# Performance work log

Hardware: AMD Instinct MI355X
Metric: run time of the kernel (lower is better)

Reference implementation:

```python
import jax, jax.numpy as jnp
import numpy as np

B, C, H = 2, 32, 64  # batch, base channel, bottleneck spatial size
EPS = 1e-5


def _conv(x, w, b, pad):
    # standard NCHW conv, stride 1
    out = jax.lax.conv_general_dilated(x, w, (1, 1), [(pad, pad), (pad, pad)],
                                       dimension_numbers=("NCHW", "OIHW", "NCHW"))
    return out + b[None, :, None, None]


def _inorm(x):
    # InstanceNorm2d, affine=False (torch default)
    m = jnp.mean(x, axis=(2, 3), keepdims=True)
    v = jnp.var(x, axis=(2, 3), keepdims=True)
    return (x - m) * jax.lax.rsqrt(v + EPS)


def _patches3(x):
    # x: (B,C,H,W) -> (B,C,9,H-2,W-2); 3x3 patches, stride 1, VALID
    oh, ow = x.shape[-2] - 2, x.shape[-1] - 2
    return jnp.stack([x[:, :, i:i + oh, j:j + ow] for i in range(3) for j in range(3)], axis=2)


def _pac_kernel(g):
    # gaussian pixel-adaptive kernel (NVlabs/pac, kernel_type='gaussian', normalize_kernel=False)
    # g: (B,Cg,H,W) -> K: (B,9,H,W), K = exp(-0.5*||f_nbr - f_center||^2)
    gp = jnp.pad(g, ((0, 0), (0, 0), (1, 1), (1, 1)))
    p = _patches3(gp)                      # (B,Cg,9,H,W)
    d = p - g[:, :, None]                  # center is offset (1,1) == g itself
    return jnp.exp(-0.5 * jnp.sum(d * d, axis=1))


def _pacconvT(x, g, w, b):
    # PacConvTranspose2d: kernel_size=3, stride=2, padding=1, output_padding=1
    # native impl: zero-upsample, pad (k-1)-p=1 left/top and 1+out_pad=2 right/bottom,
    # then pixel-adaptive conv with weight.permute(1,0,2,3) (no spatial flip, per PAC).
    Bc, Cin, Hh, Ww = x.shape
    z = jnp.zeros((Bc, Cin, 2 * Hh - 1, 2 * Ww - 1), x.dtype).at[:, :, ::2, ::2].set(x)
    z = jnp.pad(z, ((0, 0), (0, 0), (1, 2), (1, 2)))
    p = _patches3(z)                       # (B,Cin,9,2H,2W)
    k = _pac_kernel(g)                     # (B,9,2H,2W)
    wf = jnp.transpose(w, (1, 0, 2, 3)).reshape(w.shape[1], w.shape[0], 9)  # (Cout,Cin,9)
    out = jnp.einsum('bckhw,bkhw,ock->bohw', p, k, wf)
    return out + b[None, :, None, None]


def _w(key, shape, scale):
    return jax.random.normal(key, shape, dtype=jnp.float32) * scale


def setup_inputs():
    key = jax.random.key(0)
    ks = jax.random.split(key, 20)
    return {
        "x": jax.random.normal(ks[0], (B, 8 * C, H, H), jnp.float32),
        "ef_lv2": jax.random.normal(ks[1], (B, 2 * C, 2 * H, 2 * H), jnp.float32),
        "ef_lv1": jax.random.normal(ks[2], (B, C, 4 * H, 4 * H), jnp.float32),
        "W_down": _w(ks[3], (4 * C, 8 * C, 3, 3), (8 * C * 9) ** -0.5),
        "b_down": _w(ks[4], (4 * C,), 0.01),
        "W_mid": _w(ks[5], (4 * C, 4 * C, 1, 1), (4 * C) ** -0.5),
        "b_mid": _w(ks[6], (4 * C,), 0.01),
        "W_adj2": _w(ks[7], (4 * C, 2 * C, 3, 3), 0.002),  # small: keeps gaussian kernel non-degenerate
        "b_adj2": _w(ks[8], (4 * C,), 0.01),
        "W_adj1": _w(ks[9], (2 * C, C, 3, 3), 0.004),
        "b_adj1": _w(ks[10], (2 * C,), 0.01),
        "W16": _w(ks[11], (4 * C, 2 * C, 3, 3), (4 * C * 9) ** -0.5),  # convT layout (Cin,Cout,kh,kw)
        "b16": _w(ks[12], (2 * C,), 0.01),
        "W20": _w(ks[13], (2 * C, C, 3, 3), (2 * C * 9) ** -0.5),
        "b20": _w(ks[14], (C,), 0.01),
        "W24": _w(ks[15], (3, C, 3, 3), (C * 9) ** -0.5),
        "b24": _w(ks[16], (3,), 0.01),
    }


def reference(x, ef_lv2, ef_lv1, W_down, b_down, W_mid, b_mid, W_adj2, b_adj2,
              W_adj1, b_adj1, W16, b16, W20, b20, W24, b24):
    x = _conv(_inorm(x), W_down, b_down, 1)          # layer13: norm + channel-down 8C->4C
    x = _conv(x, W_mid, b_mid, 0) + x                # middle_layer13 1x1 + residual
    g2 = _conv(ef_lv2, W_adj2, b_adj2, 1)            # adjust_ef_lv2 2C->4C
    x = _pacconvT(x, g2, W16, b16)                   # layer16: 4C->2C, x2 spatial
    x = _inorm(x) + x                                # layer17 + residual (twice)
    x = _inorm(x) + x
    g1 = _conv(ef_lv1, W_adj1, b_adj1, 1)            # adjust_ef_lv1 C->2C
    x = _pacconvT(x, g1, W20, b20)                   # layer20: 2C->C, x2 spatial
    x = _inorm(x) + x                                # layer21 + residual (twice)
    x = _inorm(x) + x
    return _conv(x, W24, b24, 1)                     # layer24: C->3
```

## Files before the change

### kernel.cpp

```cpp
#include <hip/hip_runtime.h>

#define EPS 1e-5f

typedef short sh8 __attribute__((ext_vector_type(8)));
typedef float f32x4 __attribute__((ext_vector_type(4)));

__device__ __forceinline__ ushort f2b(float f) {
    unsigned u = __float_as_uint(f);
    u += 0x7fffu + ((u >> 16) & 1u);
    return (ushort)(u >> 16);
}
__device__ __forceinline__ float b2f(ushort u) {
    return __uint_as_float((unsigned)u << 16);
}

__device__ __forceinline__ void istat_body(int ch, const float* __restrict__ in,
                                           float* st, int HW)
{
    __shared__ double sh[512];
    const float* p = in + (size_t)ch * HW;
    double s = 0.0, s2 = 0.0;
    for (int i = threadIdx.x * 4; i < HW; i += 1024) {
        float4 v = *(const float4*)(p + i);
        s  += (double)v.x + (double)v.y + (double)v.z + (double)v.w;
        s2 += (double)v.x * v.x + (double)v.y * v.y
            + (double)v.z * v.z + (double)v.w * v.w;
    }
    sh[threadIdx.x] = s; sh[256 + threadIdx.x] = s2;
    __syncthreads();
    for (int o = 128; o > 0; o >>= 1) {
        if ((int)threadIdx.x < o) {
            sh[threadIdx.x]       += sh[threadIdx.x + o];
            sh[256 + threadIdx.x] += sh[256 + threadIdx.x + o];
        }
        __syncthreads();
    }
    if (threadIdx.x == 0) {
        double m = sh[0] / (double)HW;
        double v = sh[256] / (double)HW - m * m;
        st[2 * ch]     = (float)m;
        st[2 * ch + 1] = (float)(v < 0.0 ? 0.0 : v);
    }
}

__device__ __forceinline__ void ipad_body(int bxi, int b,
    const float* __restrict__ in, const float* __restrict__ st,
    ushort* __restrict__ ob, int C, int H, int W, int pad, int n4)
{
    int idx = bxi * 256 + threadIdx.x;
    if (idx >= n4) return;
    int cpp = C >> 2;
    int pp = idx / cpp, c0 = (idx - pp * cpp) * 4;
    int Wp = W + 2 * pad, Hp = H + 2 * pad;
    int yp = pp / Wp, xp = pp - yp * Wp;
    int y = yp - pad, x = xp - pad;
    ushort4 o;
    if (y >= 0 && y < H && x >= 0 && x < W) {
        size_t HW = (size_t)H * W;
        const float* ib = in + (size_t)b * C * HW + (size_t)y * W + x;
        #pragma unroll
        for (int u = 0; u < 4; u++) {
            int chg = b * C + c0 + u;
            float m = st[2 * chg];
            float inv = rsqrtf(st[2 * chg + 1] + EPS);
            float v = ib[(size_t)(c0 + u) * HW];
            ((ushort*)&o)[u] = f2b((v - m) * inv);
        }
    } else { o.x = o.y = o.z = o.w = 0; }
    *(ushort4*)(ob + ((size_t)b * Hp * Wp + pp) * C + c0) = o;
}

__device__ __forceinline__ void pad_body(int bxi, int b,
    const float* __restrict__ in, ushort* __restrict__ ob,
    int C, int H, int W, int pad, int n4)
{
    int idx = bxi * 256 + threadIdx.x;
    if (idx >= n4) return;
    int cpp = C >> 2;
    int pp = idx / cpp, c0 = (idx - pp * cpp) * 4;
    int Wp = W + 2 * pad, Hp = H + 2 * pad;
    int yp = pp / Wp, xp = pp - yp * Wp;
    int y = yp - pad, x = xp - pad;
    ushort4 o;
    if (y >= 0 && y < H && x >= 0 && x < W) {
        const float* ib = in + ((size_t)b * C) * H * W + (size_t)y * W + x;
        size_t HW = (size_t)H * W;
        o.x = f2b(ib[(size_t)(c0    ) * HW]);
        o.y = f2b(ib[(size_t)(c0 + 1) * HW]);
        o.z = f2b(ib[(size_t)(c0 + 2) * HW]);
        o.w = f2b(ib[(size_t)(c0 + 3) * HW]);
    } else { o.x = o.y = o.z = o.w = 0; }
    *(ushort4*)(ob + ((size_t)b * Hp * Wp + pp) * C + c0) = o;
}

__device__ __forceinline__ void wprep_body(int bxi,
    const float* W16, const float* W20, const float* Wd, const float* Wa2,
    const float* Wa1,
    ushort* wT1b, ushort* wT2b, ushort* wbD, ushort* wbA2b, ushort* wbA1b)
{
    int idx = bxi * 256 + threadIdx.x;
    if (idx < 73728) {
        int to = idx / 128, ci = idx - to * 128;
        int t = to / 64, o = to - t * 64;
        wT1b[idx] = f2b(W16[((size_t)ci * 64 + o) * 9 + t]);
        return;
    } idx -= 73728;
    if (idx < 18432) {
        int to = idx / 64, ci = idx - to * 64;
        int t = to / 32, o = to - t * 32;
        wT2b[idx] = f2b(W20[((size_t)ci * 32 + o) * 9 + t]);
        return;
    } idx -= 18432;
    if (idx < 294912) {
        int co = idx / 2304, r = idx - co * 2304;
        int t = r / 256, ci = r - t * 256;
        wbD[idx] = f2b(Wd[((size_t)co * 256 + ci) * 9 + t]);
        return;
    } idx -= 294912;
    if (idx < 73728) {
        int co = idx / 576, r = idx - co * 576;
        int t = r / 64, ci = r - t * 64;
        wbA2b[idx] = f2b(Wa2[((size_t)co * 64 + ci) * 9 + t]);
        return;
    } idx -= 73728;
    if (idx < 18432) {
        int co = idx / 288, r = idx - co * 288;
        int t = r / 32, ci = r - t * 32;
        wbA1b[idx] = f2b(Wa1[((size_t)co * 32 + ci) * 9 + t]);
        return;
    }
}

template<int CI, int TAPS, int KCH, int CPB, int OUTB>
__device__ __forceinline__ void mg2f_body(int bx, int by, int bz,
    const ushort* __restrict__ inb, const ushort* __restrict__ wb,
    const float* __restrict__ bias, void* __restrict__ outp,
    int wshift, int Wp, int NS, size_t SS,
    size_t in_bstride, size_t out_bstride, int HW, ushort* bsm)
{
    constexpr int CPBSH = (CPB == 1) ? 0 : (CPB == 2) ? 1 : 2;
    constexpr int SPR   = TAPS * CPB;
    constexpr int TOT   = TAPS * KCH;
    constexpr int PS    = SPR * 32 + 8;

    int b = bz / NS, sl = bz - b * NS;
    int cilo = sl * (KCH * 32);
    int tid = threadIdx.x;
    int wv = tid >> 6, l = tid & 63;
    int lane16 = l & 15, quad = l >> 4;
    int klane = quad * 8;
    int pb = bx * 128 + wv * 32;
    int nb0 = by * 32;

    int base[2];
    #pragma unroll
    for (int i = 0; i < 2; i++) {
        int pm = pb + i * 16 + lane16;
        if (TAPS == 9) {
            int W = 1 << wshift;
            int y = pm >> wshift, xx = pm & (W - 1);
            base[i] = (y + 1) * Wp + (xx + 1);
        } else base[i] = pm;
    }
    int nn[2];
    nn[0] = nb0 + lane16; nn[1] = nb0 + 16 + lane16;

    const ushort* inbb = inb + (size_t)b * in_bstride + cilo + klane;
    const ushort* wbs  = wb + cilo;
    const ushort* bp0 = bsm + lane16 * PS + klane;
    const ushort* bp1 = bsm + (16 + lane16) * PS + klane;

    f32x4 vz = {0.f, 0.f, 0.f, 0.f};
    f32x4 acc[2][2] = {{vz, vz}, {vz, vz}};
    sh8 A[3][2];

    #define LDA(ss, av) { \
        int r_ = (ss) / SPR; int l_ = (ss) - r_ * SPR; \
        int t_ = l_ >> CPBSH; int ch_ = r_ * CPB + (l_ & (CPB - 1)); \
        int dof_ = 0; \
        if (TAPS == 9) { \
            int dy_ = (t_ * 43) >> 7; \
            int dx_ = t_ - dy_ * 3; \
            dof_ = (dy_ - 1) * Wp + (dx_ - 1); \
        } \
        int coff_ = ch_ << 5; \
        av[0] = *(const sh8*)(inbb + (size_t)(base[0] + dof_) * CI + coff_); \
        av[1] = *(const sh8*)(inbb + (size_t)(base[1] + dof_) * CI + coff_); \
    }

    LDA(0, A[0])
    if (TOT > 1) LDA(1, A[1])

    #pragma unroll
    for (int r = 0; r < KCH / CPB; r++) {
        if (r) __syncthreads();
        {
            constexpr int elems = 32 * SPR * 4;
            for (int j = tid; j < elems; j += 256) {
                int n  = j / (SPR * 4);
                int rr = j - n * (SPR * 4);
                int kc = rr >> 2, c8 = rr & 3;
                int t_ = kc >> CPBSH, co = kc & (CPB - 1);
                int ch_ = r * CPB + co;
                sh8 v = *(const sh8*)(wbs
                    + ((size_t)(nb0 + n) * TAPS + t_) * CI + (ch_ << 5) + (c8 << 3));
                *(sh8*)(bsm + n * PS + (kc << 5) + (c8 << 3)) = v;
            }
        }
        __syncthreads();
        #pragma unroll
        for (int li = 0; li < SPR; li++) {
            const int s = r * SPR + li;
            if (s + 2 < TOT) LDA(s + 2, A[(s + 2) % 3])
            sh8 b0 = *(const sh8*)(bp0 + (li << 5));
            sh8 b1 = *(const sh8*)(bp1 + (li << 5));
            acc[0][0] = __builtin_amdgcn_mfma_f32_16x16x32_bf16(A[s % 3][0], b0, acc[0][0], 0, 0, 0);
            acc[0][1] = __builtin_amdgcn_mfma_f32_16x16x32_bf16(A[s % 3][0], b1, acc[0][1], 0, 0, 0);
            acc[1][0] = __builtin_amdgcn_mfma_f32_16x16x32_bf16(A[s % 3][1], b0, acc[1][0], 0, 0, 0);
            acc[1][1] = __builtin_amdgcn_mfma_f32_16x16x32_bf16(A[s % 3][1], b1, acc[1][1], 0, 0, 0);
        }
    }
    #undef LDA

    #pragma unroll
    for (int j = 0; j < 2; j++) {
        float bb = bias ? bias[nn[j]] : 0.f;
        #pragma unroll
        for (int i = 0; i < 2; i++) {
            int p0 = pb + i * 16 + quad * 4;
            if (OUTB) {
                ushort* ob = (ushort*)outp + (size_t)sl * SS + (size_t)b * out_bstride;
                ushort4 ov;
                ov.x = f2b(acc[i][j][0] + bb); ov.y = f2b(acc[i][j][1] + bb);
                ov.z = f2b(acc[i][j][2] + bb); ov.w = f2b(acc[i][j][3] + bb);
                *(ushort4*)(ob + (size_t)nn[j] * HW + p0) = ov;
            } else {
                float* ob = (float*)outp + (size_t)sl * SS + (size_t)b * out_bstride;
                *(float4*)(ob + (size_t)nn[j] * HW + p0) =
                    make_float4(acc[i][j][0] + bb, acc[i][j][1] + bb,
                                acc[i][j][2] + bb, acc[i][j][3] + bb);
            }
        }
    }
}

__device__ __forceinline__ void pack4_body(int bxi, int zy,
    const ushort* __restrict__ g, float* __restrict__ part,
    int Cg, int CS, int H, int W, int NS, size_t SS)
{
    int b = zy / NS, sl = zy - b * NS;
    int WC = W >> 2;
    int idx = bxi * 256 + threadIdx.x;
    int y = idx / WC, xc = idx - y * WC;
    int x0 = xc << 2;
    bool lz = (x0 == 0), rz = (x0 + 4 == W);
    float acc[9][4];
    #pragma unroll
    for (int t = 0; t < 9; t++)
        #pragma unroll
        for (int p = 0; p < 4; p++) acc[t][p] = 0.f;

    const ushort* gb = g + ((size_t)b * Cg + sl * CS) * H * W;
    for (int ci = 0; ci < CS; ci++) {
        const ushort* gc = gb + (size_t)ci * H * W;
        float e[3][6];
        #pragma unroll
        for (int r = 0; r < 3; r++) {
            int yy = y + r - 1;
            float4 v = make_float4(0.f, 0.f, 0.f, 0.f);
            if (yy >= 0 && yy < H) {
                ushort4 u = *(const ushort4*)(gc + (size_t)yy * W + x0);
                v = make_float4(b2f(u.x), b2f(u.y), b2f(u.z), b2f(u.w));
            }
            float lf = __shfl_up(v.w, 1);
            float rt = __shfl_down(v.x, 1);
            e[r][0] = lz ? 0.f : lf;
            e[r][1] = v.x; e[r][2] = v.y; e[r][3] = v.z; e[r][4] = v.w;
            e[r][5] = rz ? 0.f : rt;
        }
        #pragma unroll
        for (int i = 0; i < 3; i++)
            #pragma unroll
            for (int j = 0; j < 3; j++)
                #pragma unroll
                for (int p = 0; p < 4; p++) {
                    float d = e[i][p + j] - e[1][p + 1];
                    acc[i * 3 + j][p] = fmaf(d, d, acc[i * 3 + j][p]);
                }
    }
    size_t HW = (size_t)H * W;
    #pragma unroll
    for (int t = 0; t < 9; t++) {
        float4 o;
        if (NS == 1) {
            o = make_float4(expf(-0.5f * acc[t][0]), expf(-0.5f * acc[t][1]),
                            expf(-0.5f * acc[t][2]), expf(-0.5f * acc[t][3]));
        } else {
            o = make_float4(acc[t][0], acc[t][1], acc[t][2], acc[t][3]);
        }
        *(float4*)(part + (size_t)sl * SS + ((size_t)b * 9 + t) * HW
                   + (size_t)y * W + x0) = o;
    }
}

__device__ __forceinline__ void reduce_body(int bxi,
    const float* __restrict__ part, const float* __restrict__ bias,
    const float* res, float* out, int HW, int Co, int NS, size_t SS)
{
    int i4 = (bxi * 256 + threadIdx.x) * 4;
    float4 a = make_float4(0.f, 0.f, 0.f, 0.f);
    for (int s = 0; s < NS; s++) {
        float4 p = *(const float4*)(part + (size_t)s * SS + i4);
        a.x += p.x; a.y += p.y; a.z += p.z; a.w += p.w;
    }
    int c = (i4 / HW) % Co;
    float bb = bias[c];
    if (res) {
        float4 r = *(const float4*)(res + i4);
        a.x += r.x; a.y += r.y; a.z += r.z; a.w += r.w;
    }
    *(float4*)(out + i4) = make_float4(a.x + bb, a.y + bb, a.z + bb, a.w + bb);
}

__device__ __forceinline__ void expcomb_body(int bxi,
    const float* __restrict__ part, float* __restrict__ K, int NS, size_t SS)
{
    int i4 = (bxi * 256 + threadIdx.x) * 4;
    float4 a = make_float4(0.f, 0.f, 0.f, 0.f);
    for (int s = 0; s < NS; s++) {
        float4 p = *(const float4*)(part + (size_t)s * SS + i4);
        a.x += p.x; a.y += p.y; a.z += p.z; a.w += p.w;
    }
    *(float4*)(K + i4) = make_float4(expf(-0.5f * a.x), expf(-0.5f * a.y),
                                     expf(-0.5f * a.z), expf(-0.5f * a.w));
}

__global__ __launch_bounds__(256) void pro_k(
    const float* x, const float* ef2, const float* ef1,
    const float* W16, const float* W20, const float* Wd, const float* Wa2,
    const float* Wa1,
    ushort* wT1b, ushort* wT2b, ushort* wbD, ushort* wbA2b, ushort* wbA1b,
    float* st0, ushort* padA2b, ushort* padA1b)
{
    int bid = blockIdx.x;
    if (bid < 1872) {
        wprep_body(bid, W16, W20, Wd, Wa2, Wa1, wT1b, wT2b, wbD, wbA2b, wbA1b);
        return;
    } bid -= 1872;
    if (bid < 512) { istat_body(bid, x, st0, 4096); return; } bid -= 512;
    if (bid < 2114) {
        pad_body(bid % 1057, bid / 1057, ef2, padA2b, 64, 128, 128, 1, 270400);
        return;
    } bid -= 2114;
    pad_body(bid % 2081, bid / 2081, ef1, padA1b, 32, 256, 256, 1, 532512);
}

__global__ __launch_bounds__(256) void l1_k(
    const float* x, const float* st0, ushort* padDb,
    const ushort* padA2b, const ushort* wbA2b, const float* ba2, ushort* g2,
    const ushort* padA1b, const ushort* wbA1b, const float* ba1, ushort* g1)
{
    __shared__ ushort smem[32 * (9 * 32 + 8)];
    int bid = blockIdx.x;
    if (bid < 1024) {
        mg2f_body<64, 9, 2, 1, 1>(bid & 127, (bid >> 7) & 3, bid >> 9,
            padA2b, wbA2b, ba2, g2, 7, 130, 1, (size_t)0,
            (size_t)1081600, (size_t)2097152, 16384, smem);
        return;
    } bid -= 1024;
    if (bid < 2048) {
        mg2f_body<32, 9, 1, 1, 1>(bid & 511, (bid >> 9) & 1, bid >> 10,
            padA1b, wbA1b, ba1, g1, 8, 258, 1, (size_t)0,
            (size_t)2130048, (size_t)4194304, 65536, smem);
        return;
    } bid -= 2048;
    ipad_body(bid % 1089, bid / 1089, x, st0, padDb, 256, 64, 64, 1, 278784);
}

__global__ __launch_bounds__(256) void l2_k(
    const ushort* padDb, const ushort* wbD, float* Pd,
    const ushort* g1, float* PK1, const ushort* g2, float* PK2)
{
    __shared__ ushort smem[32 * (9 * 32 + 8)];
    int bid = blockIdx.x;
    if (bid < 512) {
        pack4_body(bid & 63, bid >> 6, g1, PK1, 64, 16, 256, 256, 4, (size_t)1179648);
        return;
    } bid -= 512;
    if (bid < 256) {
        pack4_body(bid & 15, bid >> 4, g2, PK2, 128, 16, 128, 128, 8, (size_t)294912);
        return;
    } bid -= 256;
    mg2f_body<256, 9, 1, 1, 0>(bid & 31, (bid >> 5) & 3, bid >> 7,
        padDb, wbD, nullptr, Pd, 6, 66, 8, (size_t)1048576,
        (size_t)1115136, (size_t)524288, 4096, smem);
}

__global__ __launch_bounds__(256) void l3_k(
    const float* Pd, const float* bd, float* x1,
    const float* PK1, float* K1, const float* PK2, float* K2, double* sta)
{
    int bid = blockIdx.x;
    if (bid == 0) {
        for (int t = threadIdx.x; t < 384; t += 256) sta[t] = 0.0;
    }
    if (bid < 1024) {
        reduce_body(bid, Pd, bd, nullptr, x1, 4096, 128, 8, (size_t)1048576);
        return;
    } bid -= 1024;
    if (bid < 1152) {
        expcomb_body(bid, PK1, K1, 4, (size_t)1179648);
        return;
    } bid -= 1152;
    expcomb_body(bid, PK2, K2, 8, (size_t)294912);
}

__global__ __launch_bounds__(256) void conv1x1f_k(
    const float* __restrict__ x1, const float* __restrict__ Wm,
    const float* __restrict__ bm, ushort* __restrict__ x2b)
{
    __shared__ float wsm[512];
    int b = blockIdx.z;
    int co0 = blockIdx.y * 4;
    int tid = threadIdx.x;
    for (int j = tid; j < 512; j += 256) {
        int co = j >> 7, ci = j & 127;
        wsm[j] = Wm[(size_t)(co0 + co) * 128 + ci];
    }
    __syncthreads();
    int px0 = (blockIdx.x * 256 + tid) * 4;
    const float* ib = x1 + (size_t)b * 524288 + px0;
    float acc[4][4];
    #pragma unroll
    for (int j = 0; j < 4; j++)
        #pragma unroll
        for (int p = 0; p < 4; p++) acc[j][p] = 0.f;
    for (int ci = 0; ci < 128; ci++) {
        float4 v = *(const float4*)(ib + (size_t)ci * 4096);
        #pragma unroll
        for (int j = 0; j < 4; j++) {
            float wv = wsm[j * 128 + ci];
            acc[j][0] = fmaf(v.x, wv, acc[j][0]);
            acc[j][1] = fmaf(v.y, wv, acc[j][1]);
            acc[j][2] = fmaf(v.z, wv, acc[j][2]);
            acc[j][3] = fmaf(v.w, wv, acc[j][3]);
        }
    }
    float vals[4][4];
    #pragma unroll
    for (int j = 0; j < 4; j++) {
        float4 r = *(const float4*)(ib + (size_t)(co0 + j) * 4096);
        float bb = bm[co0 + j];
        vals[0][j] = acc[j][0] + r.x + bb;
        vals[1][j] = acc[j][1] + r.y + bb;
        vals[2][j] = acc[j][2] + r.z + bb;
        vals[3][j] = acc[j][3] + r.w + bb;
    }
    #pragma unroll
    for (int p = 0; p < 4; p++) {
        ushort4 ov;
        ov.x = f2b(vals[p][0]); ov.y = f2b(vals[p][1]);
        ov.z = f2b(vals[p][2]); ov.w = f2b(vals[p][3]);
        *(ushort4*)(x2b + ((size_t)b * 4096 + px0 + p) * 128 + co0) = ov;
    }
}

template<int CI, int TAPS, int KCH, int CPB, int OUTB>
__global__ __launch_bounds__(256) void mg2f_k(
    const ushort* __restrict__ inb, const ushort* __restrict__ wb,
    const float* __restrict__ bias, void* __restrict__ outp,
    int wshift, int Wp, int NS, size_t SS,
    size_t in_bstride, size_t out_bstride, int HW)
{
    constexpr int PS = TAPS * CPB * 32 + 8;
    __shared__ ushort smem[32 * PS];
    mg2f_body<CI, TAPS, KCH, CPB, OUTB>(blockIdx.x, blockIdx.y, blockIdx.z,
        inb, wb, bias, outp, wshift, Wp, NS, SS, in_bstride, out_bstride, HW, smem);
}

__global__ __launch_bounds__(256) void iapad_k(const float* __restrict__ in,
    const double* __restrict__ sta, ushort* __restrict__ ob, int HW, int Co)
{
    int i4 = (blockIdx.x * 256 + threadIdx.x) * 4;
    int ch = i4 / HW;
    int p = i4 - ch * HW;
    int b = ch / Co, c = ch - b * Co;
    double S = sta[2 * ch], S2 = sta[2 * ch + 1];
    double md = S / (double)HW;
    double vr = S2 / (double)HW - md * md;
    float m = (float)md;
    float inv = rsqrtf((float)(vr < 0.0 ? 0.0 : vr) + EPS);
    float4 v = *(const float4*)(in + i4);
    ushort* op = ob + ((size_t)b * HW + p) * Co + c;
    op[0]              = f2b(v.x + 2.f * (v.x - m) * inv);
    op[(size_t)Co]     = f2b(v.y + 2.f * (v.y - m) * inv);
    op[(size_t)Co * 2] = f2b(v.z + 2.f * (v.z - m) * inv);
    op[(size_t)Co * 3] = f2b(v.w + 2.f * (v.w - m) * inv);
}

template<int NCO>
__global__ __launch_bounds__(256) void conv3x3_d(const float* __restrict__ in,
    const float* __restrict__ w, const float* __restrict__ bias,
    float* __restrict__ outp, const double* __restrict__ sta,
    int Ci, int CS, int H, int W, int Co, int NS, size_t SS)
{
    int z = blockIdx.z;
    int b = z / NS, sl = z - b * NS;
    int WC = W >> 2;
    int idx = blockIdx.x * 256 + threadIdx.x;
    int xc = idx % WC, y = idx / WC;
    int x0 = xc << 2;
    bool lz = (x0 == 0), rz = (x0 + 4 == W);
    int co0 = blockIdx.y * NCO;
    float acc[NCO][4];
    #pragma unroll
    for (int j = 0; j < NCO; j++)
        #pragma unroll
        for (int p = 0; p < 4; p++) acc[j][p] = 0.f;

    const float* ib = in + ((size_t)b * Ci + sl * CS) * H * W;
    for (int ci = 0; ci < CS; ci++) {
        const float* ic = ib + (size_t)ci * H * W;
        int cig = sl * CS + ci;
        float sa = 1.f, sb = 0.f;
        if (sta) {
            int chg = b * Ci + cig;
            double S = sta[2 * chg], S2 = sta[2 * chg + 1];
            double n = (double)H * W;
            double md = S / n;
            double vr = S2 / n - md * md;
            float inv = rsqrtf((float)(vr < 0.0 ? 0.0 : vr) + EPS);
            sa = 1.f + 2.f * inv;
            sb = -2.f * (float)md * inv;
        }
        float e[3][6];
        #pragma unroll
        for (int r = 0; r < 3; r++) {
            int yy = y + r - 1;
            float4 v = make_float4(0.f, 0.f, 0.f, 0.f);
            if (yy >= 0 && yy < H) {
                v = *(const float4*)(ic + (size_t)yy * W + x0);
                if (sta) {
                    v.x = fmaf(v.x, sa, sb); v.y = fmaf(v.y, sa, sb);
                    v.z = fmaf(v.z, sa, sb); v.w = fmaf(v.w, sa, sb);
                }
            }
            float lf = __shfl_up(v.w, 1);
            float rt = __shfl_down(v.x, 1);
            e[r][0] = lz ? 0.f : lf;
            e[r][1] = v.x; e[r][2] = v.y; e[r][3] = v.z; e[r][4] = v.w;
            e[r][5] = rz ? 0.f : rt;
        }
        #pragma unroll
        for (int j = 0; j < NCO; j++) {
            const float* wj = w + ((size_t)(co0 + j) * Ci + cig) * 9;
            #pragma unroll
            for (int r = 0; r < 3; r++) {
                float w0 = wj[3 * r], w1 = wj[3 * r + 1], w2 = wj[3 * r + 2];
                #pragma unroll
                for (int p = 0; p < 4; p++)
                    acc[j][p] = fmaf(e[r][p], w0,
                                fmaf(e[r][p + 1], w1,
                                fmaf(e[r][p + 2], w2, acc[j][p])));
            }
        }
    }
    size_t HW = (size_t)H * W;
    #pragma unroll
    for (int j = 0; j < NCO; j++) {
        float bb = bias ? bias[co0 + j] : 0.f;
        float4 o = make_float4(acc[j][0] + bb, acc[j][1] + bb,
                               acc[j][2] + bb, acc[j][3] + bb);
        float* op = outp + (size_t)sl * SS
                  + ((size_t)b * Co + co0 + j) * HW + (size_t)y * W + x0;
        *(float4*)op = o;
    }
}

__global__ __launch_bounds__(256) void reduce_k(const float* __restrict__ part,
    const float* __restrict__ bias, const float* res, float* out,
    int HW, int Co, int NS, size_t SS)
{
    reduce_body(blockIdx.x, part, bias, res, out, HW, Co, NS, SS);
}

template<int NCO>
__global__ __launch_bounds__(256) void pacsc_k(const ushort* __restrict__ Gin,
    const float* __restrict__ K, const float* __restrict__ bias,
    float* __restrict__ out, double* __restrict__ sta,
    int Cout, int Hi, int Wi, size_t gstride)
{
    int b = blockIdx.z;
    int H = Hi << 1, W = Wi << 1;
    int HW = H * W, HWi = Hi * Wi, WC = W >> 2;
    int idx = blockIdx.x * 256 + threadIdx.x;
    int half = (H >> 1) * WC;
    int py = (idx >= half) ? 1 : 0;
    int r = idx - py * half;
    int ry = r / WC;
    int y = 2 * ry + py;
    int x0 = (r - ry * WC) << 2;
    int yi = y >> 1, xi0 = x0 >> 1;
    int co0 = blockIdx.y * NCO;
    const ushort* G  = Gin + (size_t)b * gstride;
    const float* Kb = K + (size_t)b * 9 * HW;
    float* ob = out + (size_t)b * Cout * HW;
    size_t krow = (size_t)y * W + x0;
    bool vok = (xi0 + 2 < Wi);

    double ts[NCO], ts2[NCO];
    #pragma unroll
    for (int j = 0; j < NCO; j++) { ts[j] = 0.0; ts2[j] = 0.0; }

    if (py == 0) {
        float k4a = Kb[(size_t)4 * HW + krow],     k4b = Kb[(size_t)4 * HW + krow + 2];
        float k3a = Kb[(size_t)3 * HW + krow + 1], k3b = Kb[(size_t)3 * HW + krow + 3];
        float k5a = Kb[(size_t)5 * HW + krow + 1], k5b = Kb[(size_t)5 * HW + krow + 3];
        #pragma unroll
        for (int j = 0; j < NCO; j++) {
            int co = co0 + j;
            size_t rowb = (size_t)yi * Wi + xi0;
            const ushort* g3 = G + (size_t)(3 * Cout + co) * HWi + rowb;
            const ushort* g4 = G + (size_t)(4 * Cout + co) * HWi + rowb;
            const ushort* g5 = G + (size_t)(5 * Cout + co) * HWi + rowb;
            float bb = bias[co];
            float g5b = vok ? b2f(g5[2]) : 0.f;
            float o0 = fmaf(k4a, b2f(g4[0]), bb);
            float o1 = fmaf(k3a, b2f(g3[0]), fmaf(k5a, b2f(g5[1]), bb));
            float o2 = fmaf(k4b, b2f(g4[1]), bb);
            float o3 = fmaf(k3b, b2f(g3[1]), fmaf(k5b, g5b, bb));
            *(float4*)(ob + (size_t)co * HW + krow) = make_float4(o0, o1, o2, o3);
            ts[j]  += (double)o0 + o1 + o2 + o3;
            ts2[j] += (double)o0 * o0 + (double)o1 * o1
                    + (double)o2 * o2 + (double)o3 * o3;
        }
    } else {
        bool yok = (yi + 1 < Hi);
        float k1a = Kb[(size_t)1 * HW + krow],     k1b = Kb[(size_t)1 * HW + krow + 2];
        float k7a = Kb[(size_t)7 * HW + krow],     k7b = Kb[(size_t)7 * HW + krow + 2];
        float k0a = Kb[(size_t)0 * HW + krow + 1], k0b = Kb[(size_t)0 * HW + krow + 3];
        float k2a = Kb[(size_t)2 * HW + krow + 1], k2b = Kb[(size_t)2 * HW + krow + 3];
        float k6a = Kb[(size_t)6 * HW + krow + 1], k6b = Kb[(size_t)6 * HW + krow + 3];
        float k8a = Kb[(size_t)8 * HW + krow + 1], k8b = Kb[(size_t)8 * HW + krow + 3];
        #pragma unroll
        for (int j = 0; j < NCO; j++) {
            int co = co0 + j;
            size_t row0 = (size_t)yi * Wi + xi0;
            size_t row1 = (size_t)(yi + 1) * Wi + xi0;
            const ushort* g0 = G + (size_t)(0 * Cout + co) * HWi + row0;
            const ushort* g1 = G + (size_t)(1 * Cout + co) * HWi + row0;
            const ushort* g2 = G + (size_t)(2 * Cout + co) * HWi + row0;
            const ushort* g6 = G + (size_t)(6 * Cout + co) * HWi + row1;
            const ushort* g7 = G + (size_t)(7 * Cout + co) * HWi + row1;
            const ushort* g8 = G + (size_t)(8 * Cout + co) * HWi + row1;
            float bb = bias[co];
            float g2b = vok ? b2f(g2[2]) : 0.f;
            float g6a = yok ? b2f(g6[0]) : 0.f, g6b = yok ? b2f(g6[1]) : 0.f;
            float g7a = yok ? b2f(g7[0]) : 0.f, g7b = yok ? b2f(g7[1]) : 0.f;
            float g8a = yok ? b2f(g8[1]) : 0.f;
            float g8b = (yok && vok) ? b2f(g8[2]) : 0.f;
            float o0 = fmaf(k1a, b2f(g1[0]), fmaf(k7a, g7a, bb));
            float o1 = fmaf(k0a, b2f(g0[0]), fmaf(k2a, b2f(g2[1]),
                       fmaf(k6a, g6a, fmaf(k8a, g8a, bb))));
            float o2 = fmaf(k1b, b2f(g1[1]), fmaf(k7b, g7b, bb));
            float o3 = fmaf(k0b, b2f(g0[1]), fmaf(k2b, g2b,
                       fmaf(k6b, g6b, fmaf(k8b, g8b, bb))));
            *(float4*)(ob + (size_t)co * HW + krow) = make_float4(o0, o1, o2, o3);
            ts[j]  += (double)o0 + o1 + o2 + o3;
            ts2[j] += (double)o0 * o0 + (double)o1 * o1
                    + (double)o2 * o2 + (double)o3 * o3;
        }
    }

    __shared__ double sred[8];
    int l = threadIdx.x & 63, wv = threadIdx.x >> 6;
    #pragma unroll
    for (int j = 0; j < NCO; j++) {
        double s = ts[j], s2 = ts2[j];
        for (int off = 32; off > 0; off >>= 1) {
            s  += __shfl_down(s, off);
            s2 += __shfl_down(s2, off);
        }
        if (l == 0) { sred[wv] = s; sred[4 + wv] = s2; }
        __syncthreads();
        if (threadIdx.x == 0) {
            double S  = sred[0] + sred[1] + sred[2] + sred[3];
            double S2 = sred[4] + sred[5] + sred[6] + sred[7];
            int co = co0 + j;
            atomicAdd(&sta[(size_t)(b * Cout + co) * 2],     S);
            atomicAdd(&sta[(size_t)(b * Cout + co) * 2 + 1], S2);
        }
        __syncthreads();
    }
}

extern "C" void kernel_launch(void* const* d_in, const int* in_sizes, int n_in,
                              void* d_out, int out_size, void* d_ws, size_t ws_size,
                              hipStream_t stream)
{
    const float* x   = (const float*)d_in[0];
    const float* ef2 = (const float*)d_in[1];
    const float* ef1 = (const float*)d_in[2];
    const float* Wd  = (const float*)d_in[3];
    const float* bd  = (const float*)d_in[4];
    const float* Wm  = (const float*)d_in[5];
    const float* bm  = (const float*)d_in[6];
    const float* Wa2 = (const float*)d_in[7];
    const float* ba2 = (const float*)d_in[8];
    const float* Wa1 = (const float*)d_in[9];
    const float* ba1 = (const float*)d_in[10];
    const float* W16 = (const float*)d_in[11];
    const float* b16 = (const float*)d_in[12];
    const float* W20 = (const float*)d_in[13];
    const float* b20 = (const float*)d_in[14];
    const float* W24 = (const float*)d_in[15];
    const float* b24 = (const float*)d_in[16];
    float* out = (float*)d_out;

    float* P = (float*)d_ws;
    size_t o = 0;
    auto take = [&](size_t n) { float* p = P + o; o += n; return p; };
    ushort* padDb  = (ushort*)take(1115136);
    ushort* wbD    = (ushort*)take(147456);
    float*  Pd     = take(8388608);
    float*  x1     = take(1048576);
    ushort* x2b    = (ushort*)take(524288);
    ushort* padA2b = (ushort*)take(1081600);
    ushort* wbA2b  = (ushort*)take(36864);
    ushort* g2     = (ushort*)take(2097152);
    float*  PK2    = take(2359296);
    float*  K2     = take(294912);
    ushort* Gin1   = (ushort*)take(2359296);
    float*  x3     = take(2097152);
    ushort* x3b    = (ushort*)take(1048576);
    ushort* padA1b = (ushort*)take(2130048);
    ushort* wbA1b  = (ushort*)take(9216);
    ushort* g1     = (ushort*)take(4194304);
    float*  PK1    = take(4718592);
    float*  K1     = take(1179648);
    ushort* Gin2   = (ushort*)take(4718592);
    float*  x5     = take(4194304);
    float*  Pf     = take(1572864);
    ushort* wT1b   = (ushort*)take(36864);
    ushort* wT2b   = (ushort*)take(9216);
    float*  ST     = take(1024);
    double* STA    = (double*)take(768);
    float* st0 = ST;

    pro_k<<<dim3(8660), dim3(256), 0, stream>>>(
        x, ef2, ef1, W16, W20, Wd, Wa2, Wa1,
        wT1b, wT2b, wbD, wbA2b, wbA1b, st0, padA2b, padA1b);

    l1_k<<<dim3(5250), dim3(256), 0, stream>>>(
        x, st0, padDb, padA2b, wbA2b, ba2, g2, padA1b, wbA1b, ba1, g1);

    l2_k<<<dim3(2816), dim3(256), 0, stream>>>(
        padDb, wbD, Pd, g1, PK1, g2, PK2);

    l3_k<<<dim3(2464), dim3(256), 0, stream>>>(Pd, bd, x1, PK1, K1, PK2, K2, STA);

    conv1x1f_k<<<dim3(4, 32, 2), dim3(256), 0, stream>>>(x1, Wm, bm, x2b);

    mg2f_k<128, 1, 4, 4, 1><<<dim3(32, 18, 2), dim3(256), 0, stream>>>(
        x2b, wT1b, nullptr, Gin1, 0, 0, 1, (size_t)0,
        (size_t)524288, (size_t)2359296, 4096);
    pacsc_k<2><<<dim3(16, 32, 2), dim3(256), 0, stream>>>(
        Gin1, K2, b16, x3, STA, 64, 64, 64, (size_t)2359296);

    iapad_k<<<dim3(2048), dim3(256), 0, stream>>>(x3, STA, x3b, 16384, 64);

    mg2f_k<64, 1, 2, 2, 1><<<dim3(128, 9, 2), dim3(256), 0, stream>>>(
        x3b, wT2b, nullptr, Gin2, 0, 0, 1, (size_t)0,
        (size_t)1048576, (size_t)4718592, 16384);
    pacsc_k<2><<<dim3(64, 16, 2), dim3(256), 0, stream>>>(
        Gin2, K1, b20, x5, STA + 256, 32, 128, 128, (size_t)4718592);

    conv3x3_d<3><<<dim3(64, 1, 8), dim3(256), 0, stream>>>(
        x5, W24, nullptr, Pf, STA + 256, 32, 8, 256, 256, 3, 4, (size_t)393216);
    reduce_k<<<dim3(384), dim3(256), 0, stream>>>(Pf, b24, nullptr, out, 65536, 3, 4, 393216);
}
```

Baseline: 305.6 us.

## Stage shared input halo tile in LDS for 3x3 convs instead of per-tap loads

Adds a new implicit-GEMM conv body that loads one halo input tile (R rows by Wt columns by 32 channels) into shared memory per channel chunk and reads all 9 taps from it at shifted offsets. The three 3x3 convolutions (the two guide-adjust convs and the channel-down conv) now use it in place of the generic per-tap staging. The aim is to cut redundant global loads of overlapping 3x3 patches. In exchange each block uses more shared memory, which may lower occupancy.

After: 296.8 us. 1.03x faster.

```diff
diff --git a/kernel.cpp b/kernel.cpp
--- a/kernel.cpp
+++ b/kernel.cpp
@@ -131,6 +131,101 @@
     }
 }
 
+template<int CI, int KCH, int WSH, int R, int Wt, int OUTB>
+__device__ __forceinline__ void mg2s9_body(int bx, int by, int bz,
+    const ushort* __restrict__ inb, const ushort* __restrict__ wb,
+    const float* __restrict__ bias, void* __restrict__ outp,
+    int NS, size_t SS, size_t in_bstride, size_t out_bstride, ushort* sm)
+{
+    constexpr int W  = 1 << WSH;
+    constexpr int Wp = W + 2;
+    constexpr int HW = 1 << (2 * WSH);
+    constexpr int ABASE = R * Wt * 32;
+    constexpr int PS = 9 * 32 + 8;
+
+    int b = bz / NS, sl = bz - b * NS;
+    int cilo = sl * (KCH * 32);
+    int tid = threadIdx.x;
+    int wv = tid >> 6, l = tid & 63;
+    int lane16 = l & 15, quad = l >> 4;
+    int klane = quad * 8;
+    int pb = bx * 128 + wv * 32;
+    int nb0 = by * 32;
+    int ty0 = (bx * 128) >> WSH;
+    int cx0 = (bx * 128) & (W - 1) & ~127;
+
+    int al[2], nn[2];
+    #pragma unroll
+    for (int i = 0; i < 2; i++) {
+        int pm = pb + i * 16 + lane16;
+        int y = pm >> WSH, xx = pm & (W - 1);
+        al[i] = ((quad * R + (y - ty0)) * Wt + (xx - cx0)) * 8;
+    }
+    nn[0] = nb0 + lane16; nn[1] = nb0 + 16 + lane16;
+
+    const ushort* asrc0 = inb + (size_t)b * in_bstride + cilo;
+    const ushort* wbs   = wb + cilo;
+    ushort* smB = sm + ABASE;
+    const ushort* bp0 = smB + lane16 * PS + klane;
+    const ushort* bp1 = smB + (16 + lane16) * PS + klane;
+
+    f32x4 vz = {0.f, 0.f, 0.f, 0.f};
+    f32x4 acc[2][2] = {{vz, vz}, {vz, vz}};
+
+    #pragma unroll
+    for (int r = 0; r < KCH; r++) {
+        if (r) __syncthreads();
+        for (int j = tid; j < 32 * 9 * 4; j += 256) {
+            int n = j / 36, rr = j - n * 36;
+            int t_ = rr >> 2, c8 = rr & 3;
+            sh8 v = *(const sh8*)(wbs
+                + ((size_t)(nb0 + n) * 9 + t_) * CI + (r << 5) + (c8 << 3));
+            *(sh8*)(smB + n * PS + (t_ << 5) + (c8 << 3)) = v;
+        }
+        for (int j = tid; j < R * Wt * 4; j += 256) {
+            int g = j >> 2, q = j & 3;
+            int rowl = g / Wt, coll = g - rowl * Wt;
+            sh8 v = *(const sh8*)(asrc0
+                + ((size_t)(ty0 + rowl) * Wp + cx0 + coll) * CI + (r << 5) + (q << 3));
+            *(sh8*)(sm + ((q * R + rowl) * Wt + coll) * 8) = v;
+        }
+        __syncthreads();
+        #pragma unroll
+        for (int t = 0; t < 9; t++) {
+            const int aoff = ((t / 3) * Wt + (t % 3)) * 8;
+            sh8 a0 = *(const sh8*)(sm + al[0] + aoff);
+            sh8 a1 = *(const sh8*)(sm + al[1] + aoff);
+            sh8 b0 = *(const sh8*)(bp0 + (t << 5));
+            sh8 b1 = *(const sh8*)(bp1 + (t << 5));
+            acc[0][0] = __builtin_amdgcn_mfma_f32_16x16x32_bf16(a0, b0, acc[0][0], 0, 0, 0);
+            acc[0][1] = __builtin_amdgcn_mfma_f32_16x16x32_bf16(a0, b1, acc[0][1], 0, 0, 0);
+            acc[1][0] = __builtin_amdgcn_mfma_f32_16x16x32_bf16(a1, b0, acc[1][0], 0, 0, 0);
+            acc[1][1] = __builtin_amdgcn_mfma_f32_16x16x32_bf16(a1, b1, acc[1][1], 0, 0, 0);
+        }
+    }
+
+    #pragma unroll
+    for (int j = 0; j < 2; j++) {
+        float bb = bias ? bias[nn[j]] : 0.f;
+        #pragma unroll
+        for (int i = 0; i < 2; i++) {
+            int p0 = pb + i * 16 + quad * 4;
+            if (OUTB) {
+                ushort* ob = (ushort*)outp + (size_t)sl * SS + (size_t)b * out_bstride;
+                ushort4 ov;
+                ov.x = f2b(acc[i][j][0] + bb); ov.y = f2b(acc[i][j][1] + bb);
+                ov.z = f2b(acc[i][j][2] + bb); ov.w = f2b(acc[i][j][3] + bb);
+                *(ushort4*)(ob + (size_t)nn[j] * HW + p0) = ov;
+            } else {
+                float* ob = (float*)outp + (size_t)sl * SS + (size_t)b * out_bstride;
+                *(float4*)(ob + (size_t)nn[j] * HW + p0) =
+                    make_float4(acc[i][j][0] + bb, acc[i][j][1] + bb,
+                                acc[i][j][2] + bb, acc[i][j][3] + bb);
+            }
+        }
+    }
+}
+
 template<int CI, int TAPS, int KCH, int CPB, int OUTB>
 __device__ __forceinline__ void mg2f_body(int bx, int by, int bz,
     const ushort* __restrict__ inb, const ushort* __restrict__ wb,
@@ -360,18 +455,18 @@
     const ushort* padA2b, const ushort* wbA2b, const float* ba2, ushort* g2,
     const ushort* padA1b, const ushort* wbA1b, const float* ba1, ushort* g1)
 {
-    __shared__ ushort smem[32 * (9 * 32 + 8)];
+    __shared__ ushort smem[21952];
     int bid = blockIdx.x;
     if (bid < 1024) {
-        mg2f_body<64, 9, 2, 1, 1>(bid & 127, (bid >> 7) & 3, bid >> 9,
-            padA2b, wbA2b, ba2, g2, 7, 130, 1, (size_t)0,
-            (size_t)1081600, (size_t)2097152, 16384, smem);
+        mg2s9_body<64, 2, 7, 3, 130, 1>(bid & 127, (bid >> 7) & 3, bid >> 9,
+            padA2b, wbA2b, ba2, g2, 1, (size_t)0,
+            (size_t)1081600, (size_t)2097152, smem);
         return;
     } bid -= 1024;
     if (bid < 2048) {
-        mg2f_body<32, 9, 1, 1, 1>(bid & 511, (bid >> 9) & 1, bid >> 10,
-            padA1b, wbA1b, ba1, g1, 8, 258, 1, (size_t)0,
-            (size_t)2130048, (size_t)4194304, 65536, smem);
+        mg2s9_body<32, 1, 8, 3, 130, 1>(bid & 511, (bid >> 9) & 1, bid >> 10,
+            padA1b, wbA1b, ba1, g1, 1, (size_t)0,
+            (size_t)2130048, (size_t)4194304, smem);
         return;
     } bid -= 2048;
     ipad_body(bid % 1089, bid / 1089, x, st0, padDb, 256, 64, 64, 1, 278784);
@@ -381,7 +476,7 @@
     const ushort* padDb, const ushort* wbD, float* Pd,
     const ushort* g1, float* PK1, const ushort* g2, float* PK2)
 {
-    __shared__ ushort smem[32 * (9 * 32 + 8)];
+    __shared__ ushort smem[17920];
     int bid = blockIdx.x;
     if (bid < 512) {
         pack4_body(bid & 63, bid >> 6, g1, PK1, 64, 16, 256, 256, 4, (size_t)1179648);
@@ -391,9 +486,9 @@
         pack4_body(bid & 15, bid >> 4, g2, PK2, 128, 16, 128, 128, 8, (size_t)294912);
         return;
     } bid -= 256;
-    mg2f_body<256, 9, 1, 1, 0>(bid & 31, (bid >> 5) & 3, bid >> 7,
-        padDb, wbD, nullptr, Pd, 6, 66, 8, (size_t)1048576,
-        (size_t)1115136, (size_t)524288, 4096, smem);
+    mg2s9_body<256, 1, 6, 4, 66, 0>(bid & 31, (bid >> 5) & 3, bid >> 7,
+        padDb, wbD, nullptr, Pd, 8, (size_t)1048576,
+        (size_t)1115136, (size_t)524288, smem);
 }
 
 __global__ __launch_bounds__(256) void l3_k(
```
